# Optimization experiments

Measured on AMD Instinct MI355X. Metric: run time of the kernel, lower is better.

Reference implementation:

```python
import jax, jax.numpy as jnp
import numpy as np

B, E, S, H = 4, 1024, 1024, 16
HD = E // H  # head_size = 64
MASK_VALUE = -1000000000.0
W_SCALE = 0.05  # keep pre-softmax logits moderate since original softmax is not max-stabilized


def setup_inputs() -> dict:
    key = jax.random.key(0)
    ks = jax.random.split(key, 7)
    queries = jax.random.normal(ks[0], (B, E, S), jnp.float32)
    keys = jax.random.normal(ks[1], (B, E, S), jnp.float32)
    values = jax.random.normal(ks[2], (B, E, S), jnp.float32)
    # causal multiplicative mask, broadcast over batch
    mask = jnp.broadcast_to(jnp.tril(jnp.ones((S, S), jnp.float32)), (B, S, S))
    Wq = jax.random.normal(ks[3], (H, HD, HD), jnp.float32) * W_SCALE
    Wk = jax.random.normal(ks[4], (H, HD, HD), jnp.float32) * W_SCALE
    Wv = jax.random.normal(ks[5], (H, HD, HD), jnp.float32) * W_SCALE
    Wf = jax.random.normal(ks[6], (E, E), jnp.float32) * W_SCALE
    return dict(queries=queries, keys=keys, values=values, mask=mask,
                Wq=Wq, Wk=Wk, Wv=Wv, Wf=Wf)


def reference(queries, keys, values, mask, Wq, Wk, Wv, Wf):
    # channels-first: [B, E, S] -> split embedding axis into heads: [B, H, HD, S]
    qh = queries.reshape(B, H, HD, S)
    kh = keys.reshape(B, H, HD, S)
    vh = values.reshape(B, H, HD, S)
    # per-head linear projections: W[h] @ x_slice, batched over heads
    q = jnp.einsum('hde,bhes->bhds', Wq, qh)
    k = jnp.einsum('hde,bhes->bhds', Wk, kh)
    v = jnp.einsum('hde,bhes->bhds', Wv, vh)
    # pre_softmax = Q^T @ K / sqrt(head_size)  -> [B, H, S, S]
    pre = jnp.einsum('bhds,bhdt->bhst', q, k) / jnp.sqrt(jnp.float32(HD))
    m = mask[:, None, :, :]  # broadcast mask over heads
    pre = pre * m + (m == 0).astype(jnp.float32) * MASK_VALUE
    # Faithful to original: exp / reduce_sum(axis=-1)[..., None, :]
    # i.e. post[b,h,i,j] = exp(pre[b,h,i,j]) / sum_t exp(pre[b,h,j,t])
    e = jnp.exp(pre)
    post = e / jnp.sum(e, axis=3)[:, :, None, :]
    # values @ post^T : out[b,h,d,i] = sum_j v[b,h,d,j] * post[b,h,i,j]
    out_h = jnp.einsum('bhdj,bhij->bhdi', v, post)
    pre_linear = out_h.reshape(B, E, S)  # concat heads along embedding axis
    return jnp.einsum('ef,bfs->bes', Wf, pre_linear)
```

## Files before the change

kernel.cpp:

```cpp
#include <hip/hip_runtime.h>
#include <hip/hip_bf16.h>
#include <stdint.h>

#define NB 4
#define NH 16
#define HDIM 64
#define NS 1024
#define NE 1024

typedef __bf16 bf16x8 __attribute__((ext_vector_type(8)));
typedef __bf16 bf16x2_t __attribute__((ext_vector_type(2)));
typedef float f32x4 __attribute__((ext_vector_type(4)));
typedef unsigned int uint4v __attribute__((ext_vector_type(4)));
typedef unsigned int uint2v __attribute__((ext_vector_type(2)));
typedef unsigned short u16;

#if defined(__has_builtin)
#if __has_builtin(__builtin_amdgcn_global_load_lds)
#define HAVE_GLDS 1
#endif
#endif

__device__ __forceinline__ u16 f2bf(float f) {
  return __builtin_bit_cast(u16, (__bf16)f);
}
__device__ __forceinline__ unsigned pk2(float a, float b) {
  bf16x2_t v; v[0] = (__bf16)a; v[1] = (__bf16)b;
  return __builtin_bit_cast(unsigned, v);
}
__device__ __forceinline__ float fexp2(float x) {
#if defined(__has_builtin)
#if __has_builtin(__builtin_amdgcn_exp2f)
  return __builtin_amdgcn_exp2f(x);
#else
  return __expf(x * 0.69314718056f);
#endif
#else
  return __expf(x * 0.69314718056f);
#endif
}
__device__ __forceinline__ f32x4 mfma16(bf16x8 a, bf16x8 b, f32x4 c) {
  return __builtin_amdgcn_mfma_f32_16x16x32_bf16(a, b, c, 0, 0, 0);
}
__device__ __forceinline__ bf16x8 ld_bf8(const u16* p) {
  return __builtin_bit_cast(bf16x8, *(const uint4v*)p);
}
#ifdef HAVE_GLDS
__device__ __forceinline__ void gld16(const void* g, void* l) {
  __builtin_amdgcn_global_load_lds(
      (__attribute__((address_space(1))) void*)g,
      (__attribute__((address_space(3))) void*)l, 16, 0, 0);
}
#endif

__global__ __launch_bounds__(256) void proj_kernel(
    const float* __restrict__ q_in, const float* __restrict__ k_in,
    const float* __restrict__ v_in, const float* __restrict__ Wq,
    const float* __restrict__ Wk, const float* __restrict__ Wv,
    const float* __restrict__ Wf,
    u16* __restrict__ qT, u16* __restrict__ kT, u16* __restrict__ vv,
    u16* __restrict__ Wf16)
{
  const int which = blockIdx.z;
  const int tid = threadIdx.x;

  if (which == 3) {
    int chunk = blockIdx.y * 4 + blockIdx.x;
    #pragma unroll
    for (int jj = 0; jj < 4; ++jj) {
      int i = chunk * 1024 + tid + 256 * jj;
      float4 f = ((const float4*)Wf)[i];
      uint2v p;
      p[0] = pk2(f.x, f.y);
      p[1] = pk2(f.z, f.w);
      ((uint2v*)Wf16)[i] = p;
    }
    return;
  }

  const int bh = blockIdx.y;
  const int b = bh >> 4, h = bh & 15;
  const int s0 = blockIdx.x * 256;
  const int w = tid >> 6, l = tid & 63, lr = l & 15, lg = l >> 4;

  const float* x = (which == 0) ? q_in : (which == 1) ? k_in : v_in;
  const float* W = ((which == 0) ? Wq : (which == 1) ? Wk : Wv) + h * 4096;
  const float wsc = (which == 0) ? 0.18033688f : 1.0f;

  __shared__ alignas(16) u16 xT[256][72];
  __shared__ alignas(16) u16 Wl[64][72];

  #pragma unroll
  for (int j = 0; j < 4; ++j) {
    int i = tid * 4 + j;
    int d = i >> 4;
    int e0 = (i & 15) * 4;
    float4 f = *(const float4*)(W + d * 64 + e0);
    uint2v p;
    p[0] = pk2(f.x * wsc, f.y * wsc);
    p[1] = pk2(f.z * wsc, f.w * wsc);
    *(uint2v*)&Wl[d][e0] = p;
  }
  {
    const float* xp = x + ((size_t)b * NE + h * 64) * NS + s0 + tid;
    #pragma unroll
    for (int j = 0; j < 8; ++j) {
      uint4v pk;
      #pragma unroll
      for (int q = 0; q < 4; ++q) {
        float f0 = xp[(size_t)(j * 8 + q * 2) * NS];
        float f1 = xp[(size_t)(j * 8 + q * 2 + 1) * NS];
        pk[q] = pk2(f0, f1);
      }
      *(uint4v*)&xT[tid][j * 8] = pk;
    }
  }
  __syncthreads();

  bf16x8 af[4][2];
  #pragma unroll
  for (int mt = 0; mt < 4; ++mt) {
    af[mt][0] = ld_bf8(&Wl[mt * 16 + lr][lg * 8]);
    af[mt][1] = ld_bf8(&Wl[mt * 16 + lr][32 + lg * 8]);
  }
  f32x4 acc[4][4] = {};
  #pragma unroll
  for (int nt = 0; nt < 4; ++nt) {
    bf16x8 b0 = ld_bf8(&xT[w * 64 + nt * 16 + lr][lg * 8]);
    bf16x8 b1 = ld_bf8(&xT[w * 64 + nt * 16 + lr][32 + lg * 8]);
    #pragma unroll
    for (int mt = 0; mt < 4; ++mt) {
      acc[mt][nt] = mfma16(af[mt][0], b0, acc[mt][nt]);
      acc[mt][nt] = mfma16(af[mt][1], b1, acc[mt][nt]);
    }
  }

  if (which < 2) {
    u16* o = ((which == 0) ? qT : kT) + (size_t)bh * NS * 64;
    #pragma unroll
    for (int mt = 0; mt < 4; ++mt)
      #pragma unroll
      for (int nt = 0; nt < 4; ++nt) {
        int s = s0 + w * 64 + nt * 16 + lr;
        int d = mt * 16 + lg * 4;
        uint2v p;
        p[0] = pk2(acc[mt][nt][0], acc[mt][nt][1]);
        p[1] = pk2(acc[mt][nt][2], acc[mt][nt][3]);
        *(uint2v*)(o + (size_t)s * 64 + d) = p;
      }
  } else {
    u16* o = vv + (size_t)bh * 64 * NS;
    #pragma unroll
    for (int mt = 0; mt < 4; ++mt)
      #pragma unroll
      for (int nt = 0; nt < 4; ++nt)
        #pragma unroll
        for (int jr = 0; jr < 4; ++jr) {
          int d = mt * 16 + lg * 4 + jr;
          int s = s0 + w * 64 + nt * 16 + lr;
          o[(size_t)d * NS + s] = f2bf(acc[mt][nt][jr]);
        }
  }
}

__global__ __launch_bounds__(512) void denom_kernel(
    const u16* __restrict__ qT, const u16* __restrict__ kT,
    float* __restrict__ l2rDg)
{
  const int wg = blockIdx.x;
  const int rt = 7 - (wg >> 6);
  const int bh = wg & 63;
  const int i0 = rt * 128;
  const int tid = threadIdx.x, w = tid >> 6, l = tid & 63, lr = l & 15, lg = l >> 4;
  __shared__ alignas(16) u16 klds[128][72];
  const u16* qb = qT + (size_t)bh * NS * 64;
  const u16* kb = kT + (size_t)bh * NS * 64;
  const int gi = i0 + w * 16 + lr;
  bf16x8 bq0 = ld_bf8(qb + (size_t)gi * 64 + lg * 8);
  bf16x8 bq1 = ld_bf8(qb + (size_t)gi * 64 + 32 + lg * 8);
  float den = 0.f;
  const int nkt = rt + 1;
  uint4v kreg[2];
  const int krow = tid >> 3, kcx = tid & 7;
  #pragma unroll
  for (int j = 0; j < 2; ++j)
    kreg[j] = *(const uint4v*)(kb + (size_t)(krow + j * 64) * 64 + kcx * 8);
  for (int t = 0; t < nkt; ++t) {
    __syncthreads();
    #pragma unroll
    for (int j = 0; j < 2; ++j)
      *(uint4v*)&klds[krow + j * 64][kcx * 8] = kreg[j];
    __syncthreads();
    const int t0 = t * 128;
    if (t + 1 < nkt) {
      #pragma unroll
      for (int j = 0; j < 2; ++j)
        kreg[j] = *(const uint4v*)(kb + (size_t)(t0 + 128 + krow + j * 64) * 64 + kcx * 8);
    }
    if (t + 1 < nkt) {
      #pragma unroll
      for (int mt = 0; mt < 8; ++mt) {
        bf16x8 a0 = ld_bf8(&klds[mt * 16 + lr][lg * 8]);
        bf16x8 a1 = ld_bf8(&klds[mt * 16 + lr][32 + lg * 8]);
        f32x4 z = {0.f, 0.f, 0.f, 0.f};
        f32x4 sc = mfma16(a0, bq0, z);
        sc = mfma16(a1, bq1, sc);
        den += fexp2(sc[0]) + fexp2(sc[1]) + fexp2(sc[2]) + fexp2(sc[3]);
      }
    } else {
      #pragma unroll
      for (int mt = 0; mt < 8; ++mt) {
        bf16x8 a0 = ld_bf8(&klds[mt * 16 + lr][lg * 8]);
        bf16x8 a1 = ld_bf8(&klds[mt * 16 + lr][32 + lg * 8]);
        f32x4 z = {0.f, 0.f, 0.f, 0.f};
        f32x4 sc = mfma16(a0, bq0, z);
        sc = mfma16(a1, bq1, sc);
        #pragma unroll
        for (int r = 0; r < 4; ++r) {
          int gt = t0 + mt * 16 + lg * 4 + r;
          den += (gt <= gi) ? fexp2(sc[r]) : 0.f;
        }
      }
    }
  }
  den += __shfl_xor(den, 16);
  den += __shfl_xor(den, 32);
  if (l < 16) l2rDg[(size_t)bh * NS + gi] = -__log2f(den);
}

__global__ __launch_bounds__(512) void attn_kernel(
    const u16* __restrict__ qT, const u16* __restrict__ kT,
    const u16* __restrict__ vv, const float* __restrict__ l2rDg,
    u16* __restrict__ X)
{
  const int wg = blockIdx.x;
  const int rt = 7 - (wg >> 6);
  const int bh = wg & 63;
  const int b = bh >> 4, h = bh & 15;
  const int i0 = rt * 128;
  const int tid = threadIdx.x, w = tid >> 6, l = tid & 63, lr = l & 15, lg = l >> 4;
  __shared__ alignas(16) u16 klds[128][72];
  __shared__ alignas(16) u16 vlds[64][136];
  __shared__ alignas(16) u16 plds[8][16][72];
  __shared__ alignas(16) float dlds[128];
  const u16* qb = qT + (size_t)bh * NS * 64;
  const u16* kb = kT + (size_t)bh * NS * 64;
  const u16* vb = vv + (size_t)bh * 64 * NS;
  const float* rb = l2rDg + (size_t)bh * NS;
  const int gi = i0 + w * 16 + lr;
  bf16x8 bq0 = ld_bf8(qb + (size_t)gi * 64 + lg * 8);
  bf16x8 bq1 = ld_bf8(qb + (size_t)gi * 64 + 32 + lg * 8);
  f32x4 acc[4] = {};
  const int nkt = rt + 1;
  uint4v kreg[2], vreg[2];
  float dreg = 0.f;
  const int krow = tid >> 3, kcx = tid & 7;
  const int vrow = tid >> 4, vcx = tid & 15;
  #pragma unroll
  for (int j = 0; j < 2; ++j) {
    kreg[j] = *(const uint4v*)(kb + (size_t)(krow + j * 64) * 64 + kcx * 8);
    vreg[j] = *(const uint4v*)(vb + (size_t)(vrow + j * 32) * NS + vcx * 8);
  }
  if (tid < 128) dreg = rb[tid];
  for (int t = 0; t < nkt; ++t) {
    __syncthreads();
    #pragma unroll
    for (int j = 0; j < 2; ++j) {
      *(uint4v*)&klds[krow + j * 64][kcx * 8] = kreg[j];
      *(uint4v*)&vlds[vrow + j * 32][vcx * 8] = vreg[j];
    }
    if (tid < 128) dlds[tid] = dreg;
    __syncthreads();
    const int t0 = t * 128;
    if (t + 1 < nkt) {
      const int t0n = t0 + 128;
      #pragma unroll
      for (int j = 0; j < 2; ++j) {
        kreg[j] = *(const uint4v*)(kb + (size_t)(t0n + krow + j * 64) * 64 + kcx * 8);
        vreg[j] = *(const uint4v*)(vb + (size_t)(vrow + j * 32) * NS + t0n + vcx * 8);
      }
      if (tid < 128) dreg = rb[t0n + tid];
    }
    const bool diag = (t + 1 == nkt);
    #pragma unroll
    for (int hh = 0; hh < 2; ++hh) {
      #pragma unroll
      for (int mt = 0; mt < 4; ++mt) {
        bf16x8 a0 = ld_bf8(&klds[hh * 64 + mt * 16 + lr][lg * 8]);
        bf16x8 a1 = ld_bf8(&klds[hh * 64 + mt * 16 + lr][32 + lg * 8]);
        f32x4 z = {0.f, 0.f, 0.f, 0.f};
        f32x4 sc = mfma16(a0, bq0, z);
        sc = mfma16(a1, bq1, sc);
        f32x4 l2 = *(const f32x4*)&dlds[hh * 64 + mt * 16 + lg * 4];
        uint2v p;
        if (!diag) {
          p[0] = pk2(fexp2(sc[0] + l2[0]), fexp2(sc[1] + l2[1]));
          p[1] = pk2(fexp2(sc[2] + l2[2]), fexp2(sc[3] + l2[3]));
        } else {
          int g0 = t0 + hh * 64 + mt * 16 + lg * 4;
          float e0 = (g0 + 0 <= gi) ? fexp2(sc[0] + l2[0]) : 0.f;
          float e1 = (g0 + 1 <= gi) ? fexp2(sc[1] + l2[1]) : 0.f;
          float e2 = (g0 + 2 <= gi) ? fexp2(sc[2] + l2[2]) : 0.f;
          float e3 = (g0 + 3 <= gi) ? fexp2(sc[3] + l2[3]) : 0.f;
          p[0] = pk2(e0, e1);
          p[1] = pk2(e2, e3);
        }
        *(uint2v*)&plds[w][lr][mt * 16 + lg * 4] = p;
      }
      bf16x8 ap0 = ld_bf8(&plds[w][lr][lg * 8]);
      bf16x8 ap1 = ld_bf8(&plds[w][lr][32 + lg * 8]);
      __builtin_amdgcn_s_setprio(1);
      #pragma unroll
      for (int nt = 0; nt < 4; ++nt) {
        bf16x8 v0 = ld_bf8(&vlds[nt * 16 + lr][hh * 64 + lg * 8]);
        bf16x8 v1 = ld_bf8(&vlds[nt * 16 + lr][hh * 64 + 32 + lg * 8]);
        acc[nt] = mfma16(ap0, v0, acc[nt]);
        acc[nt] = mfma16(ap1, v1, acc[nt]);
      }
      __builtin_amdgcn_s_setprio(0);
    }
  }
  u16* Xp = X + (size_t)b * NS * NE + h * 64;
  #pragma unroll
  for (int nt = 0; nt < 4; ++nt)
    #pragma unroll
    for (int jr = 0; jr < 4; ++jr) {
      int s = i0 + w * 16 + lg * 4 + jr;
      Xp[(size_t)s * NE + nt * 16 + lr] = f2bf(acc[nt][jr]);
    }
}

__global__ __launch_bounds__(256) void final_gemm(
    const u16* __restrict__ Wf16, const u16* __restrict__ X,
    float* __restrict__ out)
{
  const int b = blockIdx.z;
  const int e0 = blockIdx.y * 128;
  const int s0 = blockIdx.x * 128;
  const int tid = threadIdx.x, w = tid >> 6, l = tid & 63, lr = l & 15, lg = l >> 4;
  const int wm = (w >> 1) * 64, wn = (w & 1) * 64;
  __shared__ alignas(16) u16 Ald[2][128][64];
  __shared__ alignas(16) u16 Bld[2][128][64];
  const u16* Xb = X + (size_t)b * NS * NE;
  f32x4 acc[4][4] = {};

  #define FG_ISSUE(p, k0)                                                     \
    {                                                                         \
      _Pragma("unroll")                                                       \
      for (int j = 0; j < 4; ++j) {                                           \
        int c = tid + 256 * j;                                                \
        int r = c >> 3;                                                       \
        int sc_ = ((c & 7) * 16) ^ ((r & 7) << 4);                            \
        const char* ga = (const char*)(Wf16 + (size_t)(e0 + r) * NE + (k0)) + sc_; \
        const char* gb = (const char*)(Xb + (size_t)(s0 + r) * NE + (k0)) + sc_;   \
        char* la = (char*)&Ald[p][0][0] + c * 16;                             \
        char* lb = (char*)&Bld[p][0][0] + c * 16;                             \
        STAGE16(ga, la);                                                      \
        STAGE16(gb, lb);                                                      \
      }                                                                       \
    }
#ifdef HAVE_GLDS
  #define STAGE16(g, l_) gld16((g), (l_))
#else
  #define STAGE16(g, l_) (*(uint4v*)(l_) = *(const uint4v*)(g))
#endif

  FG_ISSUE(0, 0);
  __syncthreads();
  for (int t = 0; t < 16; ++t) {
    const int p = t & 1;
    if (t < 15) FG_ISSUE(p ^ 1, (t + 1) * 64);
    __builtin_amdgcn_s_setprio(1);
    #pragma unroll
    for (int kk = 0; kk < 2; ++kk) {
      bf16x8 a[4], bb[4];
      #pragma unroll
      for (int mt = 0; mt < 4; ++mt) {
        int R = wm + mt * 16 + lr;
        a[mt] = ld_bf8((const u16*)((const char*)&Ald[p][R][0] +
                                    ((kk * 64 + lg * 16) ^ ((R & 7) << 4))));
      }
      #pragma unroll
      for (int nt = 0; nt < 4; ++nt) {
        int R = wn + nt * 16 + lr;
        bb[nt] = ld_bf8((const u16*)((const char*)&Bld[p][R][0] +
                                     ((kk * 64 + lg * 16) ^ ((R & 7) << 4))));
      }
      #pragma unroll
      for (int mt = 0; mt < 4; ++mt)
        #pragma unroll
        for (int nt = 0; nt < 4; ++nt)
          acc[mt][nt] = mfma16(a[mt], bb[nt], acc[mt][nt]);
    }
    __builtin_amdgcn_s_setprio(0);
    __syncthreads();
  }
  #pragma unroll
  for (int mt = 0; mt < 4; ++mt)
    #pragma unroll
    for (int nt = 0; nt < 4; ++nt) {
      int e = e0 + wm + mt * 16 + lg * 4;
      int s = s0 + wn + nt * 16 + lr;
      float* op = out + ((size_t)b * NE + e) * NS + s;
      op[0] = acc[mt][nt][0];
      op[NS] = acc[mt][nt][1];
      op[2 * NS] = acc[mt][nt][2];
      op[3 * NS] = acc[mt][nt][3];
    }
}

extern "C" void kernel_launch(void* const* d_in, const int* in_sizes, int n_in,
                              void* d_out, int out_size, void* d_ws, size_t ws_size,
                              hipStream_t stream) {
  (void)in_sizes; (void)n_in; (void)out_size; (void)ws_size;
  const float* q_in = (const float*)d_in[0];
  const float* k_in = (const float*)d_in[1];
  const float* v_in = (const float*)d_in[2];
  const float* Wq = (const float*)d_in[4];
  const float* Wk = (const float*)d_in[5];
  const float* Wv = (const float*)d_in[6];
  const float* Wf = (const float*)d_in[7];

  u16* qT = (u16*)d_ws;
  u16* kT = qT + (size_t)NB * NH * NS * HDIM;
  u16* vv = kT + (size_t)NB * NH * NS * HDIM;
  u16* X  = vv + (size_t)NB * NH * HDIM * NS;
  u16* Wf16 = X + (size_t)NB * NS * NE;
  float* l2rD = (float*)(Wf16 + (size_t)NE * NE);

  proj_kernel<<<dim3(4, 64, 4), 256, 0, stream>>>(q_in, k_in, v_in, Wq, Wk, Wv,
                                                  Wf, qT, kT, vv, Wf16);
  denom_kernel<<<dim3(512), 512, 0, stream>>>(qT, kT, l2rD);
  attn_kernel<<<dim3(512), 512, 0, stream>>>(qT, kT, vv, l2rD, X);
  final_gemm<<<dim3(8, 8, 4), 256, 0, stream>>>(Wf16, X, (float*)d_out);
}
```

Before: 78.73 us.

## Fold softmax denominators into V and give each wave two query row blocks

```diff
diff --git a/kernel.cpp b/kernel.cpp
--- a/kernel.cpp
+++ b/kernel.cpp
@@ -163,9 +163,9 @@
   }
 }
 
-__global__ __launch_bounds__(512) void denom_kernel(
+__global__ __launch_bounds__(256) void denom_kernel(
     const u16* __restrict__ qT, const u16* __restrict__ kT,
-    float* __restrict__ l2rDg)
+    const u16* __restrict__ vv, u16* __restrict__ vvs)
 {
   const int wg = blockIdx.x;
   const int rt = 7 - (wg >> 6);
@@ -173,65 +173,95 @@
   const int i0 = rt * 128;
   const int tid = threadIdx.x, w = tid >> 6, l = tid & 63, lr = l & 15, lg = l >> 4;
   __shared__ alignas(16) u16 klds[128][72];
+  __shared__ alignas(16) float Dsh[128];
   const u16* qb = qT + (size_t)bh * NS * 64;
   const u16* kb = kT + (size_t)bh * NS * 64;
-  const int gi = i0 + w * 16 + lr;
-  bf16x8 bq0 = ld_bf8(qb + (size_t)gi * 64 + lg * 8);
-  bf16x8 bq1 = ld_bf8(qb + (size_t)gi * 64 + 32 + lg * 8);
-  float den = 0.f;
+  const int r0 = i0 + w * 32;
+  int gi[2];
+  bf16x8 bq[2][2];
+  #pragma unroll
+  for (int s = 0; s < 2; ++s) {
+    gi[s] = r0 + s * 16 + lr;
+    bq[s][0] = ld_bf8(qb + (size_t)gi[s] * 64 + lg * 8);
+    bq[s][1] = ld_bf8(qb + (size_t)gi[s] * 64 + 32 + lg * 8);
+  }
+  float den[2] = {0.f, 0.f};
   const int nkt = rt + 1;
-  uint4v kreg[2];
+  uint4v kreg[4];
   const int krow = tid >> 3, kcx = tid & 7;
   #pragma unroll
-  for (int j = 0; j < 2; ++j)
-    kreg[j] = *(const uint4v*)(kb + (size_t)(krow + j * 64) * 64 + kcx * 8);
+  for (int j = 0; j < 4; ++j)
+    kreg[j] = *(const uint4v*)(kb + (size_t)(krow + j * 32) * 64 + kcx * 8);
   for (int t = 0; t < nkt; ++t) {
     __syncthreads();
     #pragma unroll
-    for (int j = 0; j < 2; ++j)
-      *(uint4v*)&klds[krow + j * 64][kcx * 8] = kreg[j];
+    for (int j = 0; j < 4; ++j)
+      *(uint4v*)&klds[krow + j * 32][kcx * 8] = kreg[j];
     __syncthreads();
     const int t0 = t * 128;
     if (t + 1 < nkt) {
       #pragma unroll
-      for (int j = 0; j < 2; ++j)
-        kreg[j] = *(const uint4v*)(kb + (size_t)(t0 + 128 + krow + j * 64) * 64 + kcx * 8);
-    }
-    if (t + 1 < nkt) {
-      #pragma unroll
-      for (int mt = 0; mt < 8; ++mt) {
-        bf16x8 a0 = ld_bf8(&klds[mt * 16 + lr][lg * 8]);
-        bf16x8 a1 = ld_bf8(&klds[mt * 16 + lr][32 + lg * 8]);
-        f32x4 z = {0.f, 0.f, 0.f, 0.f};
-        f32x4 sc = mfma16(a0, bq0, z);
-        sc = mfma16(a1, bq1, sc);
-        den += fexp2(sc[0]) + fexp2(sc[1]) + fexp2(sc[2]) + fexp2(sc[3]);
-      }
-    } else {
-      #pragma unroll
-      for (int mt = 0; mt < 8; ++mt) {
-        bf16x8 a0 = ld_bf8(&klds[mt * 16 + lr][lg * 8]);
-        bf16x8 a1 = ld_bf8(&klds[mt * 16 + lr][32 + lg * 8]);
-        f32x4 z = {0.f, 0.f, 0.f, 0.f};
-        f32x4 sc = mfma16(a0, bq0, z);
-        sc = mfma16(a1, bq1, sc);
+      for (int j = 0; j < 4; ++j)
+        kreg[j] = *(const uint4v*)(kb + (size_t)(t0 + 128 + krow + j * 32) * 64 + kcx * 8);
+    }
+    #pragma unroll
+    for (int hh = 0; hh < 2; ++hh) {
+      const int t0h = t0 + hh * 64;
+      bool dead0 = t0h > r0 + 15, dead1 = t0h > r0 + 31;
+      bool msk0 = !dead0 && (t0h + 63 > r0), msk1 = !dead1 && (t0h + 63 > r0 + 16);
+      if (dead0 && dead1) continue;
+      #pragma unroll
+      for (int mt = 0; mt < 4; ++mt) {
+        bf16x8 a0 = ld_bf8(&klds[hh * 64 + mt * 16 + lr][lg * 8]);
+        bf16x8 a1 = ld_bf8(&klds[hh * 64 + mt * 16 + lr][32 + lg * 8]);
         #pragma unroll
-        for (int r = 0; r < 4; ++r) {
-          int gt = t0 + mt * 16 + lg * 4 + r;
-          den += (gt <= gi) ? fexp2(sc[r]) : 0.f;
+        for (int s = 0; s < 2; ++s) {
+          bool dead = s ? dead1 : dead0, msk = s ? msk1 : msk0;
+          if (dead) continue;
+          f32x4 z = {0.f, 0.f, 0.f, 0.f};
+          f32x4 sc = mfma16(a0, bq[s][0], z);
+          sc = mfma16(a1, bq[s][1], sc);
+          if (!msk) {
+            den[s] += fexp2(sc[0]) + fexp2(sc[1]) + fexp2(sc[2]) + fexp2(sc[3]);
+          } else {
+            #pragma unroll
+            for (int r = 0; r < 4; ++r) {
+              int gt = t0h + mt * 16 + lg * 4 + r;
+              den[s] += (gt <= gi[s]) ? fexp2(sc[r]) : 0.f;
+            }
+          }
         }
       }
     }
   }
-  den += __shfl_xor(den, 16);
-  den += __shfl_xor(den, 32);
-  if (l < 16) l2rDg[(size_t)bh * NS + gi] = -__log2f(den);
-}
-
-__global__ __launch_bounds__(512) void attn_kernel(
+  #pragma unroll
+  for (int s = 0; s < 2; ++s) {
+    float d = den[s];
+    d += __shfl_xor(d, 16);
+    d += __shfl_xor(d, 32);
+    if (l < 16) Dsh[w * 32 + s * 16 + lr] = 1.0f / d;
+  }
+  __syncthreads();
+  const u16* vi = vv + (size_t)bh * 64 * NS + i0;
+  u16* vo = vvs + (size_t)bh * 64 * NS + i0;
+  const int c = (tid & 15) * 8;
+  #pragma unroll
+  for (int p4 = 0; p4 < 4; ++p4) {
+    int d = p4 * 16 + (tid >> 4);
+    bf16x8 vx = ld_bf8(vi + (size_t)d * NS + c);
+    float r[8];
+    #pragma unroll
+    for (int i = 0; i < 8; ++i) r[i] = (float)vx[i] * Dsh[c + i];
+    uint4v o;
+    o[0] = pk2(r[0], r[1]); o[1] = pk2(r[2], r[3]);
+    o[2] = pk2(r[4], r[5]); o[3] = pk2(r[6], r[7]);
+    *(uint4v*)(vo + (size_t)d * NS + c) = o;
+  }
+}
+
+__global__ __launch_bounds__(256) void attn_kernel(
     const u16* __restrict__ qT, const u16* __restrict__ kT,
-    const u16* __restrict__ vv, const float* __restrict__ l2rDg,
-    u16* __restrict__ X)
+    const u16* __restrict__ vvs, u16* __restrict__ X)
 {
   const int wg = blockIdx.x;
   const int rt = 7 - (wg >> 6);
@@ -241,93 +271,114 @@
   const int tid = threadIdx.x, w = tid >> 6, l = tid & 63, lr = l & 15, lg = l >> 4;
   __shared__ alignas(16) u16 klds[128][72];
   __shared__ alignas(16) u16 vlds[64][136];
-  __shared__ alignas(16) u16 plds[8][16][72];
-  __shared__ alignas(16) float dlds[128];
+  __shared__ alignas(16) u16 plds[4][32][72];
   const u16* qb = qT + (size_t)bh * NS * 64;
   const u16* kb = kT + (size_t)bh * NS * 64;
-  const u16* vb = vv + (size_t)bh * 64 * NS;
-  const float* rb = l2rDg + (size_t)bh * NS;
-  const int gi = i0 + w * 16 + lr;
-  bf16x8 bq0 = ld_bf8(qb + (size_t)gi * 64 + lg * 8);
-  bf16x8 bq1 = ld_bf8(qb + (size_t)gi * 64 + 32 + lg * 8);
-  f32x4 acc[4] = {};
+  const u16* vb = vvs + (size_t)bh * 64 * NS;
+  const int r0 = i0 + w * 32;
+  int gi[2];
+  bf16x8 bq[2][2];
+  #pragma unroll
+  for (int s = 0; s < 2; ++s) {
+    gi[s] = r0 + s * 16 + lr;
+    bq[s][0] = ld_bf8(qb + (size_t)gi[s] * 64 + lg * 8);
+    bq[s][1] = ld_bf8(qb + (size_t)gi[s] * 64 + 32 + lg * 8);
+  }
+  f32x4 acc[2][4] = {};
   const int nkt = rt + 1;
-  uint4v kreg[2], vreg[2];
-  float dreg = 0.f;
+  uint4v kreg[4], vreg[4];
   const int krow = tid >> 3, kcx = tid & 7;
   const int vrow = tid >> 4, vcx = tid & 15;
   #pragma unroll
-  for (int j = 0; j < 2; ++j) {
-    kreg[j] = *(const uint4v*)(kb + (size_t)(krow + j * 64) * 64 + kcx * 8);
-    vreg[j] = *(const uint4v*)(vb + (size_t)(vrow + j * 32) * NS + vcx * 8);
-  }
-  if (tid < 128) dreg = rb[tid];
+  for (int j = 0; j < 4; ++j) {
+    kreg[j] = *(const uint4v*)(kb + (size_t)(krow + j * 32) * 64 + kcx * 8);
+    vreg[j] = *(const uint4v*)(vb + (size_t)(vrow + j * 16) * NS + vcx * 8);
+  }
   for (int t = 0; t < nkt; ++t) {
     __syncthreads();
     #pragma unroll
-    for (int j = 0; j < 2; ++j) {
-      *(uint4v*)&klds[krow + j * 64][kcx * 8] = kreg[j];
-      *(uint4v*)&vlds[vrow + j * 32][vcx * 8] = vreg[j];
-    }
-    if (tid < 128) dlds[tid] = dreg;
+    for (int j = 0; j < 4; ++j) {
+      *(uint4v*)&klds[krow + j * 32][kcx * 8] = kreg[j];
+      *(uint4v*)&vlds[vrow + j * 16][vcx * 8] = vreg[j];
+    }
     __syncthreads();
     const int t0 = t * 128;
     if (t + 1 < nkt) {
       const int t0n = t0 + 128;
       #pragma unroll
-      for (int j = 0; j < 2; ++j) {
-        kreg[j] = *(const uint4v*)(kb + (size_t)(t0n + krow + j * 64) * 64 + kcx * 8);
-        vreg[j] = *(const uint4v*)(vb + (size_t)(vrow + j * 32) * NS + t0n + vcx * 8);
-      }
-      if (tid < 128) dreg = rb[t0n + tid];
-    }
-    const bool diag = (t + 1 == nkt);
+      for (int j = 0; j < 4; ++j) {
+        kreg[j] = *(const uint4v*)(kb + (size_t)(t0n + krow + j * 32) * 64 + kcx * 8);
+        vreg[j] = *(const uint4v*)(vb + (size_t)(vrow + j * 16) * NS + t0n + vcx * 8);
+      }
+    }
     #pragma unroll
     for (int hh = 0; hh < 2; ++hh) {
+      const int t0h = t0 + hh * 64;
+      bool dead0 = t0h > r0 + 15, dead1 = t0h > r0 + 31;
+      bool msk0 = !dead0 && (t0h + 63 > r0), msk1 = !dead1 && (t0h + 63 > r0 + 16);
+      if (dead0 && dead1) continue;
       #pragma unroll
       for (int mt = 0; mt < 4; ++mt) {
         bf16x8 a0 = ld_bf8(&klds[hh * 64 + mt * 16 + lr][lg * 8]);
         bf16x8 a1 = ld_bf8(&klds[hh * 64 + mt * 16 + lr][32 + lg * 8]);
-        f32x4 z = {0.f, 0.f, 0.f, 0.f};
-        f32x4 sc = mfma16(a0, bq0, z);
-        sc = mfma16(a1, bq1, sc);
-        f32x4 l2 = *(const f32x4*)&dlds[hh * 64 + mt * 16 + lg * 4];
-        uint2v p;
-        if (!diag) {
-          p[0] = pk2(fexp2(sc[0] + l2[0]), fexp2(sc[1] + l2[1]));
-          p[1] = pk2(fexp2(sc[2] + l2[2]), fexp2(sc[3] + l2[3]));
-        } else {
-          int g0 = t0 + hh * 64 + mt * 16 + lg * 4;
-          float e0 = (g0 + 0 <= gi) ? fexp2(sc[0] + l2[0]) : 0.f;
-          float e1 = (g0 + 1 <= gi) ? fexp2(sc[1] + l2[1]) : 0.f;
-          float e2 = (g0 + 2 <= gi) ? fexp2(sc[2] + l2[2]) : 0.f;
-          float e3 = (g0 + 3 <= gi) ? fexp2(sc[3] + l2[3]) : 0.f;
-          p[0] = pk2(e0, e1);
-          p[1] = pk2(e2, e3);
+        #pragma unroll
+        for (int s = 0; s < 2; ++s) {
+          bool dead = s ? dead1 : dead0, msk = s ? msk1 : msk0;
+          if (dead) continue;
+          f32x4 z = {0.f, 0.f, 0.f, 0.f};
+          f32x4 sc = mfma16(a0, bq[s][0], z);
+          sc = mfma16(a1, bq[s][1], sc);
+          uint2v p;
+          if (!msk) {
+            p[0] = pk2(fexp2(sc[0]), fexp2(sc[1]));
+            p[1] = pk2(fexp2(sc[2]), fexp2(sc[3]));
+          } else {
+            int g0 = t0h + mt * 16 + lg * 4;
+            float e0 = (g0 + 0 <= gi[s]) ? fexp2(sc[0]) : 0.f;
+            float e1 = (g0 + 1 <= gi[s]) ? fexp2(sc[1]) : 0.f;
+            float e2 = (g0 + 2 <= gi[s]) ? fexp2(sc[2]) : 0.f;
+            float e3 = (g0 + 3 <= gi[s]) ? fexp2(sc[3]) : 0.f;
+            p[0] = pk2(e0, e1);
+            p[1] = pk2(e2, e3);
+          }
+          *(uint2v*)&plds[w][s * 16 + lr][mt * 16 + lg * 4] = p;
         }
-        *(uint2v*)&plds[w][lr][mt * 16 + lg * 4] = p;
-      }
-      bf16x8 ap0 = ld_bf8(&plds[w][lr][lg * 8]);
-      bf16x8 ap1 = ld_bf8(&plds[w][lr][32 + lg * 8]);
+      }
+      bf16x8 ap[2][2];
+      #pragma unroll
+      for (int s = 0; s < 2; ++s) {
+        bool dead = s ? dead1 : dead0;
+        if (!dead) {
+          ap[s][0] = ld_bf8(&plds[w][s * 16 + lr][lg * 8]);
+          ap[s][1] = ld_bf8(&plds[w][s * 16 + lr][32 + lg * 8]);
+        }
+      }
       __builtin_amdgcn_s_setprio(1);
       #pragma unroll
       for (int nt = 0; nt < 4; ++nt) {
         bf16x8 v0 = ld_bf8(&vlds[nt * 16 + lr][hh * 64 + lg * 8]);
         bf16x8 v1 = ld_bf8(&vlds[nt * 16 + lr][hh * 64 + 32 + lg * 8]);
-        acc[nt] = mfma16(ap0, v0, acc[nt]);
-        acc[nt] = mfma16(ap1, v1, acc[nt]);
+        #pragma unroll
+        for (int s = 0; s < 2; ++s) {
+          bool dead = s ? dead1 : dead0;
+          if (dead) continue;
+          acc[s][nt] = mfma16(ap[s][0], v0, acc[s][nt]);
+          acc[s][nt] = mfma16(ap[s][1], v1, acc[s][nt]);
+        }
       }
       __builtin_amdgcn_s_setprio(0);
     }
   }
   u16* Xp = X + (size_t)b * NS * NE + h * 64;
   #pragma unroll
-  for (int nt = 0; nt < 4; ++nt)
-    #pragma unroll
-    for (int jr = 0; jr < 4; ++jr) {
-      int s = i0 + w * 16 + lg * 4 + jr;
-      Xp[(size_t)s * NE + nt * 16 + lr] = f2bf(acc[nt][jr]);
-    }
+  for (int s = 0; s < 2; ++s)
+    #pragma unroll
+    for (int nt = 0; nt < 4; ++nt)
+      #pragma unroll
+      for (int jr = 0; jr < 4; ++jr) {
+        int srow = r0 + s * 16 + lg * 4 + jr;
+        Xp[(size_t)srow * NE + nt * 16 + lr] = f2bf(acc[s][nt][jr]);
+      }
 }
 
 __global__ __launch_bounds__(256) void final_gemm(
@@ -421,16 +472,16 @@
   const float* Wv = (const float*)d_in[6];
   const float* Wf = (const float*)d_in[7];
 
-  u16* qT = (u16*)d_ws;
-  u16* kT = qT + (size_t)NB * NH * NS * HDIM;
-  u16* vv = kT + (size_t)NB * NH * NS * HDIM;
-  u16* X  = vv + (size_t)NB * NH * HDIM * NS;
+  u16* qT  = (u16*)d_ws;
+  u16* kT  = qT + (size_t)NB * NH * NS * HDIM;
+  u16* vv  = kT + (size_t)NB * NH * NS * HDIM;
+  u16* vvs = vv + (size_t)NB * NH * HDIM * NS;
+  u16* X   = vvs + (size_t)NB * NH * HDIM * NS;
   u16* Wf16 = X + (size_t)NB * NS * NE;
-  float* l2rD = (float*)(Wf16 + (size_t)NE * NE);
 
   proj_kernel<<<dim3(4, 64, 4), 256, 0, stream>>>(q_in, k_in, v_in, Wq, Wk, Wv,
                                                   Wf, qT, kT, vv, Wf16);
-  denom_kernel<<<dim3(512), 512, 0, stream>>>(qT, kT, l2rD);
-  attn_kernel<<<dim3(512), 512, 0, stream>>>(qT, kT, vv, l2rD, X);
+  denom_kernel<<<dim3(512), 256, 0, stream>>>(qT, kT, vv, vvs);
+  attn_kernel<<<dim3(512), 256, 0, stream>>>(qT, kT, vvs, X);
   final_gemm<<<dim3(8, 8, 4), 256, 0, stream>>>(Wf16, X, (float*)d_out);
 }
```

After: 86.91 us. 1.1x slower.
